# Kernel optimization log

Measured on AMD Instinct MI355X. Metric: run time of the kernel, lower is better.

Reference implementation:

```python
import jax, jax.numpy as jnp
import numpy as np

N_NODES = 100_000
E_OFF = 1_000_000
HID = 32
GF = 8
NF = 8
N_LAYERS = 3


def _mlp(h, W1, b1, W2, b2):
    # Linear -> ReLU -> Linear (matches MLP([in, hidden, out]))
    return jax.nn.relu(h @ W1 + b1) @ W2 + b2


def _seg_mean(v, idx, n):
    s = jax.ops.segment_sum(v, idx, num_segments=n)
    c = jax.ops.segment_sum(jnp.ones((v.shape[0], 1), v.dtype), idx, num_segments=n)
    return s / jnp.maximum(c, 1.0)


def _graphnet(x, row, col, eattr2, g, p):
    # GraphNet with global block: edge MLP -> mean-aggregate to nodes -> node MLP -> global MLP
    eW1, eb1, eW2, eb2, nW1, nb1, nW2, nb2, gW1, gb1, gW2, gb2 = p
    n, e = x.shape[0], row.shape[0]
    gE = jnp.broadcast_to(g, (e, g.shape[1]))
    e_emb = _mlp(jnp.concatenate([gE, x[row], x[col], eattr2], axis=1), eW1, eb1, eW2, eb2)
    agg = _seg_mean(e_emb, row, n)
    gN = jnp.broadcast_to(g, (n, g.shape[1]))
    n_emb = _mlp(jnp.concatenate([gN, x, agg], axis=1), nW1, nb1, nW2, nb2)
    g_new = _mlp(jnp.concatenate([n_emb.mean(0, keepdims=True), e_emb.mean(0, keepdims=True), g], axis=1),
                 gW1, gb1, gW2, gb2)
    return e_emb, n_emb, g_new


def setup_inputs() -> dict:
    key = jax.random.key(0)
    ks = jax.random.split(key, 24)
    a = jax.random.randint(ks[0], (E_OFF,), 0, N_NODES)
    b = jax.random.randint(ks[1], (E_OFF,), 0, N_NODES)
    d = jnp.arange(N_NODES)
    l_ei = jnp.stack([jnp.concatenate([jnp.maximum(a, b), d]),
                      jnp.concatenate([jnp.minimum(a, b), d])])  # lower triangular + diag
    c = jax.random.randint(ks[2], (E_OFF,), 0, N_NODES)
    e = jax.random.randint(ks[3], (E_OFF,), 0, N_NODES)
    u_ei = jnp.stack([jnp.concatenate([jnp.minimum(c, e), d]),
                      jnp.concatenate([jnp.maximum(c, e), d])])  # upper triangular + diag
    E = E_OFF + N_NODES
    x = jax.random.normal(ks[4], (N_NODES, NF), dtype=jnp.float32)
    l_attr = jax.random.normal(ks[5], (E, 1), dtype=jnp.float32)
    u_attr = jax.random.normal(ks[6], (E, 1), dtype=jnp.float32)

    def w(k, shape):
        return (jax.random.normal(k, shape, dtype=jnp.float32) / np.sqrt(shape[-2])).astype(jnp.float32)

    e_in = GF + 2 * NF + 1 + 1  # 26 (edge attr padded to 2: skip col, zeros where absent)
    n_in = GF + 1 + NF          # 17
    g_in = NF + 1 + GF          # 17
    return {
        'x': x, 'l_edge_index': l_ei, 'u_edge_index': u_ei,
        'l_edge_attr': l_attr, 'u_edge_attr': u_attr,
        'eW1': w(ks[7], (2, N_LAYERS, e_in, HID)), 'eb1': 0.01 * jax.random.normal(ks[8], (2, N_LAYERS, HID)),
        'eW2': w(ks[9], (2, N_LAYERS, HID, 1)), 'eb2': 0.01 * jax.random.normal(ks[10], (2, N_LAYERS, 1)),
        'nW1': w(ks[11], (2, N_LAYERS, n_in, HID)), 'nb1': 0.01 * jax.random.normal(ks[12], (2, N_LAYERS, HID)),
        'nW2': w(ks[13], (2, N_LAYERS, HID, NF)), 'nb2': 0.01 * jax.random.normal(ks[14], (2, N_LAYERS, NF)),
        'gW1': w(ks[15], (2, N_LAYERS, g_in, HID)), 'gb1': 0.01 * jax.random.normal(ks[16], (2, N_LAYERS, HID)),
        'gW2': w(ks[17], (2, N_LAYERS, HID, GF)), 'gb2': 0.01 * jax.random.normal(ks[18], (2, N_LAYERS, GF)),
    }


def reference(x, l_edge_index, u_edge_index, l_edge_attr, u_edge_attr,
              eW1, eb1, eW2, eb2, nW1, nb1, nW2, nb2, gW1, gb1, gW2, gb2):
    params = (eW1, eb1, eW2, eb2, nW1, nb1, nW2, nb2, gW1, gb1, gW2, gb2)
    lr, lc = l_edge_index[0], l_edge_index[1]
    ur, uc = u_edge_index[0], u_edge_index[1]
    g = jnp.zeros((1, GF), x.dtype)
    l_e, u_e = l_edge_attr, u_edge_attr
    l_a = l_edge_attr  # skip-connection edge features (original matrix values)
    zl, zu = jnp.zeros_like(l_edge_attr), jnp.zeros_like(u_edge_attr)
    for i in range(N_LAYERS):
        p1 = tuple(w[0, i] for w in params)
        p2 = tuple(w[1, i] for w in params)
        l_in = jnp.concatenate([l_e, l_a if i != 0 else zl], axis=1)  # zeros col == no skip (block 0)
        l_e, l_n, g = _graphnet(x, lr, lc, l_in, g, p1)
        u_in = jnp.concatenate([u_e, zu], axis=1)  # l2 never has skip; padded zeros col
        u_e, u_n, g = _graphnet(l_n, ur, uc, u_in, g, p2)
        # NOTE: node embeddings are NOT carried across MP blocks in the original
    l_vals = jnp.where(lr == lc, jnp.exp(l_e[:, 0]), l_e[:, 0])
    u_vals = jnp.where(ur == uc, jnp.exp(u_e[:, 0]), u_e[:, 0])
    return jnp.concatenate([l_vals, u_vals])
```

## Files before the change

kernel.cpp:

```cpp
#include <hip/hip_runtime.h>


typedef unsigned int u32;
typedef unsigned long long u64;

#define NB_SHIFT 8
#define NB_SIZE 256
#define RSTRIDE 1104

__device__ __forceinline__ float wave_sum(float v) {
#pragma unroll
    for (int off = 32; off > 0; off >>= 1) v += __shfl_down(v, off, 64);
    return v;
}


__global__ __launch_bounds__(512) void hist_kernel(
    const int* __restrict__ lr, const int* __restrict__ ur,
    u32* __restrict__ hist, int E, int B) {
    __shared__ u32 h[512];
    const int t = threadIdx.x;
    if (t < B) h[t] = 0;
    __syncthreads();
    const int s = blockIdx.y;
    const int* rows = s ? ur : lr;
    for (int i = blockIdx.x * 512 + t; i < E; i += gridDim.x * 512)
        atomicAdd(&h[rows[i] >> NB_SHIFT], 1u);
    __syncthreads();
    if (t < B && h[t]) atomicAdd(&hist[s * B + t], h[t]);
}

__global__ __launch_bounds__(512) void scan_kernel(
    const u32* __restrict__ hist, u32* __restrict__ offs,
    u32* __restrict__ cur, int B) {
    __shared__ u32 sh[512];
    const int t = threadIdx.x;
    for (int s = 0; s < 2; ++s) {
        const u32 v = (t < B) ? hist[s * B + t] : 0u;
        sh[t] = v;
        __syncthreads();
#pragma unroll
        for (int off = 1; off < 512; off <<= 1) {
            const u32 add = (t >= off) ? sh[t - off] : 0u;
            __syncthreads();
            sh[t] += add;
            __syncthreads();
        }
        const u32 exc = sh[t] - v;
        if (t < B) {
            offs[s * (B + 1) + t] = exc;
            cur[s * B + t] = exc;
        }
        if (t == 511) offs[s * (B + 1) + B] = sh[511];
        __syncthreads();
    }
}

#define SCHUNK 4096
__global__ __launch_bounds__(512) void scatter_kernel(
    const int* __restrict__ rows, const int* __restrict__ cols,
    const float* __restrict__ attr, u32* __restrict__ cur,
    uint4* __restrict__ my, int E, int B) {
    __shared__ u32 lcnt[512], lbase[512];
    const int t = threadIdx.x;
    if (t < B) lcnt[t] = 0;
    __syncthreads();
    const int base_e = blockIdx.x * SCHUNK;
#pragma unroll
    for (int k = 0; k < SCHUNK / 512; ++k) {
        const int e = base_e + k * 512 + t;
        if (e < E) atomicAdd(&lcnt[rows[e] >> NB_SHIFT], 1u);
    }
    __syncthreads();
    if (t < B) {
        const u32 c = lcnt[t];
        lbase[t] = c ? atomicAdd(&cur[t], c) : 0u;
        lcnt[t] = 0;
    }
    __syncthreads();
#pragma unroll
    for (int k = 0; k < SCHUNK / 512; ++k) {
        const int e = base_e + k * 512 + t;
        if (e < E) {
            const int r = rows[e];
            const int b = r >> NB_SHIFT;
            const u32 pos = lbase[b] + atomicAdd(&lcnt[b], 1u);
            my[pos] = make_uint4((u32)r, (u32)cols[e], (u32)e,
                                 __float_as_uint(attr[e]));
        }
    }
}


__global__ __launch_bounds__(512) void sort_kernel(
    const uint4* __restrict__ in, u64* __restrict__ okey,
    float* __restrict__ oattr, const u32* __restrict__ offs,
    u32* __restrict__ row_offs, int E, int N) {
    __shared__ u32 cnt[NB_SIZE];
    __shared__ u32 scn[NB_SIZE];
    const int t = threadIdx.x;
    const int b = blockIdx.x;
    const u32 beg = offs[b], end = offs[b + 1];
    if (t < NB_SIZE) cnt[t] = 0;
    __syncthreads();
    for (u32 i = beg + t; i < end; i += 512)
        atomicAdd(&cnt[in[i].x & (NB_SIZE - 1)], 1u);
    __syncthreads();
    if (t < NB_SIZE) scn[t] = cnt[t];
    __syncthreads();
#pragma unroll
    for (int off = 1; off < NB_SIZE; off <<= 1) {
        u32 add = 0;
        if (t < NB_SIZE && t >= off) add = scn[t - off];
        __syncthreads();
        if (t < NB_SIZE) scn[t] += add;
        __syncthreads();
    }
    const int n0 = b << NB_SHIFT;
    if (t < NB_SIZE) {
        const u32 excl = scn[t] - cnt[t];
        if (n0 + t < N) row_offs[n0 + t] = beg + excl;
        cnt[t] = excl;
    }
    if (b == 0 && t == 0) row_offs[N] = (u32)E;
    __syncthreads();
    for (u32 i = beg + t; i < end; i += 512) {
        const uint4 r = in[i];
        const u32 pos = beg + atomicAdd(&cnt[r.x & (NB_SIZE - 1)], 1u);
        okey[pos] = ((u64)r.z << 34) | ((u64)(r.x & 0x1FFFFu) << 17) |
                    (u64)(r.y & 0x1FFFFu);
        oattr[pos] = __uint_as_float(r.w);
    }
}


template <bool GCOMP>
__global__ __launch_bounds__(256) void nodew_kernel(
    const float4* __restrict__ xf, const float* __restrict__ W1,
    const float* __restrict__ b1,
    const float* __restrict__ gprev,
    float* __restrict__ gout,
    const float* __restrict__ pebins,
    const float* __restrict__ pnbins,
    const float* __restrict__ gW1, const float* __restrict__ gb1,
    const float* __restrict__ gW2, const float* __restrict__ gb2,
    float4* __restrict__ Atab, int N, float inv_E, int cpn) {
    __shared__ float gsh[8];
    const int t = threadIdx.x;
    if constexpr (GCOMP) {
        if (t < 64) {
            float nb[8];
#pragma unroll
            for (int q = 0; q < 8; ++q) nb[q] = pnbins[t * 16 + q];
            const float eb = pebins[t];
            float gin[17];
#pragma unroll
            for (int q = 0; q < 8; ++q) {
                const float s = wave_sum(nb[q]);
                gin[q] = __shfl(s, 0, 64) / (float)N;
            }
            const float es = wave_sum(eb);
            gin[8] = __shfl(es, 0, 64) * inv_E;
#pragma unroll
            for (int k = 0; k < 8; ++k) gin[9 + k] = gprev[k];
            float hv = 0.0f;
            if (t < 32) {
                hv = gb1[t];
#pragma unroll
                for (int k = 0; k < 17; ++k)
                    hv = fmaf(gin[k], gW1[k * 32 + t], hv);
                hv = fmaxf(hv, 0.0f);
            }
#pragma unroll
            for (int q = 0; q < 8; ++q) {
                const float c = (t < 32) ? hv * gW2[t * 8 + q] : 0.0f;
                const float s = wave_sum(c);
                if (t == 0) {
                    const float gv = gb2[q] + s;
                    gsh[q] = gv;
                    if (blockIdx.x == 0) gout[q] = gv;
                }
            }
        }
    } else {
        if (t < 8) gsh[t] = gprev[t];
    }
    __syncthreads();
    const int lid = (blockIdx.x & 7) * cpn + (blockIdx.x >> 3);
    const int n = lid * 256 + t;
    if (n >= N) return;
    float gr[8];
#pragma unroll
    for (int k = 0; k < 8; ++k) gr[k] = gsh[k];
    const float4 x0 = xf[2 * (size_t)n], x1 = xf[2 * (size_t)n + 1];
    const float xs[8] = {x0.x, x0.y, x0.z, x0.w, x1.x, x1.y, x1.z, x1.w};
    float a[32];
#pragma unroll
    for (int j = 0; j < 32; ++j) {
        float v = b1[j];
#pragma unroll
        for (int k = 0; k < 8; ++k) v = fmaf(gr[k], W1[k * 32 + j], v);
        a[j] = v;
    }
    const float* __restrict__ WA = W1 + 8 * 32;
#pragma unroll
    for (int k = 0; k < 8; ++k) {
        const float v = xs[k];
#pragma unroll
        for (int j = 0; j < 32; ++j) a[j] = fmaf(v, WA[k * 32 + j], a[j]);
    }
    float4* An = Atab + 8 * (size_t)n;
#pragma unroll
    for (int q = 0; q < 8; ++q)
        An[q] = make_float4(a[4 * q], a[4 * q + 1], a[4 * q + 2], a[4 * q + 3]);
}


template <bool SKIP, bool FIRST, bool GAGG, bool VALS, bool STORE>
__global__ __launch_bounds__(256) void edge_kernel(
    const u64* __restrict__ ekey,
    const float* __restrict__ eattr,
    const float4* __restrict__ Atab,
    const float4* __restrict__ xf,
    const float* __restrict__ eprev,
    const float* __restrict__ W1,
    const float* __restrict__ W2,
    const float* __restrict__ b2,
    float* __restrict__ ebins,
    float* __restrict__ e_out,
    float* __restrict__ vals_out,
    int E, int cpx) {
    __shared__ float wpart[4];
    const int t = threadIdx.x;
    const int lid = (blockIdx.x & 7) * cpx + (blockIdx.x >> 3);
    const int i0 = lid * 256;
    if (i0 >= E) return;
    const int i = i0 + t;
    const bool valid = i < E;
    const int idx = valid ? i : i0;

    const u64 key = ekey[idx];
    const u32 c = (u32)key & 0x1FFFFu;
    const u32 r = (u32)(key >> 17) & 0x1FFFFu;
    float attr = 0.0f;
    if constexpr (FIRST || SKIP) attr = eattr[idx];
    float epv;
    if constexpr (FIRST) epv = attr;
    else epv = eprev[idx];
    const float4* __restrict__ Ar = Atab + 8 * (size_t)r;
    float h[32];
#pragma unroll
    for (int q = 0; q < 8; ++q) {
        const float4 av = Ar[q];
        h[4 * q + 0] = av.x; h[4 * q + 1] = av.y;
        h[4 * q + 2] = av.z; h[4 * q + 3] = av.w;
    }
    const float4 xc0 = xf[2 * (size_t)c], xc1 = xf[2 * (size_t)c + 1];
    const float cx[8] = {xc0.x, xc0.y, xc0.z, xc0.w,
                         xc1.x, xc1.y, xc1.z, xc1.w};
    const float* __restrict__ Wc = W1 + 16 * 32;
#pragma unroll
    for (int k = 0; k < 8; ++k) {
        const float v = cx[k];
#pragma unroll
        for (int j = 0; j < 32; ++j) h[j] = fmaf(v, Wc[k * 32 + j], h[j]);
    }
    const float* __restrict__ W24 = W1 + 24 * 32;
#pragma unroll
    for (int j = 0; j < 32; ++j) h[j] = fmaf(epv, W24[j], h[j]);
    if constexpr (SKIP) {
        const float* __restrict__ W25 = W1 + 25 * 32;
#pragma unroll
        for (int j = 0; j < 32; ++j) h[j] = fmaf(attr, W25[j], h[j]);
    }
    float out = b2[0];
#pragma unroll
    for (int j = 0; j < 32; ++j) out = fmaf(fmaxf(h[j], 0.0f), W2[j], out);

    if (valid) {
        if constexpr (STORE) e_out[i] = out;
        if constexpr (VALS) {
            const u32 eid = (u32)(key >> 34);
            vals_out[eid] = (r == c) ? expf(out) : out;
        }
    }
    if constexpr (GAGG) {
        const float s = wave_sum(valid ? out : 0.0f);
        if ((t & 63) == 0) wpart[t >> 6] = s;
        __syncthreads();
        if (t == 0)
            atomicAdd(&ebins[lid & 63],
                      wpart[0] + wpart[1] + wpart[2] + wpart[3]);
    }
}


template <bool STORE_N>
__global__ __launch_bounds__(256) void nodemlp_kernel(
    const float* __restrict__ ep,
    const u32* __restrict__ row_offs,
    const float4* __restrict__ xf,
    const float* __restrict__ g,
    const float* __restrict__ nW1, const float* __restrict__ nb1,
    const float* __restrict__ nW2, const float* __restrict__ nb2,
    float* __restrict__ n_out,
    float* __restrict__ nbins,
    int N, int cpn) {
    __shared__ float biasN[32];
    __shared__ float npart[4][8];
    const int t = threadIdx.x;
    if (t < 32) {
        float v = nb1[t];
#pragma unroll
        for (int k = 0; k < 8; ++k) v = fmaf(g[k], nW1[k * 32 + t], v);
        biasN[t] = v;
    }
    __syncthreads();
    const int lid = (blockIdx.x & 7) * cpn + (blockIdx.x >> 3);
    const int n = lid * 256 + t;
    const bool active = n < N;
    const int idx = active ? n : (N - 1);
    const u32 beg = row_offs[idx], end = row_offs[idx + 1];
    float ssum = 0.0f;
    for (u32 i = beg; i < end; ++i) ssum += ep[i];
    const float agg = ssum / fmaxf((float)(end - beg), 1.0f);
    const float4 x0 = xf[2 * (size_t)idx], x1 = xf[2 * (size_t)idx + 1];
    float in[9] = {x0.x, x0.y, x0.z, x0.w, x1.x, x1.y, x1.z, x1.w, agg};
    float h[32];
#pragma unroll
    for (int j = 0; j < 8; ++j) {
        const float4 bb = reinterpret_cast<const float4*>(biasN)[j];
        h[4 * j + 0] = bb.x; h[4 * j + 1] = bb.y;
        h[4 * j + 2] = bb.z; h[4 * j + 3] = bb.w;
    }
    const float* __restrict__ Wk = nW1 + 8 * 32;
#pragma unroll
    for (int k = 0; k < 9; ++k) {
        const float v = in[k];
#pragma unroll
        for (int j = 0; j < 32; ++j) h[j] = fmaf(v, Wk[k * 32 + j], h[j]);
    }
    float o[8];
#pragma unroll
    for (int q = 0; q < 8; ++q) o[q] = nb2[q];
#pragma unroll
    for (int j = 0; j < 32; ++j) {
        const float hv = fmaxf(h[j], 0.0f);
#pragma unroll
        for (int q = 0; q < 8; ++q) o[q] = fmaf(hv, nW2[j * 8 + q], o[q]);
    }
    if constexpr (STORE_N) {
        if (active) {
            reinterpret_cast<float4*>(n_out)[2 * n] =
                make_float4(o[0], o[1], o[2], o[3]);
            reinterpret_cast<float4*>(n_out)[2 * n + 1] =
                make_float4(o[4], o[5], o[6], o[7]);
        }
    }
#pragma unroll
    for (int q = 0; q < 8; ++q) {
        const float s2 = wave_sum(active ? o[q] : 0.0f);
        if ((t & 63) == 0) npart[t >> 6][q] = s2;
    }
    __syncthreads();
    if (t < 8) {
        float a = 0.0f;
#pragma unroll
        for (int w = 0; w < 4; ++w) a += npart[w][t];
        atomicAdd(&nbins[(blockIdx.x & 63) * 16 + t], a);
    }
}

extern "C" void kernel_launch(void* const* d_in, const int* in_sizes, int n_in,
                              void* d_out, int out_size, void* d_ws,
                              size_t ws_size, hipStream_t stream) {
    const float* x = (const float*)d_in[0];
    const int* l_ei = (const int*)d_in[1];
    const int* u_ei = (const int*)d_in[2];
    const float* l_attr = (const float*)d_in[3];
    const float* u_attr = (const float*)d_in[4];
    const float* eW1 = (const float*)d_in[5];
    const float* eb1 = (const float*)d_in[6];
    const float* eW2 = (const float*)d_in[7];
    const float* eb2 = (const float*)d_in[8];
    const float* nW1 = (const float*)d_in[9];
    const float* nb1 = (const float*)d_in[10];
    const float* nW2 = (const float*)d_in[11];
    const float* nb2 = (const float*)d_in[12];
    const float* gW1 = (const float*)d_in[13];
    const float* gb1 = (const float*)d_in[14];
    const float* gW2 = (const float*)d_in[15];
    const float* gb2 = (const float*)d_in[16];

    const int E = in_sizes[3];
    const int N = in_sizes[0] / 8;
    const int B = (N + NB_SIZE - 1) >> NB_SHIFT;
    const int Ep = (E + 3) & ~3;

    u64* ekeys = (u64*)d_ws;
    float* eattrs = (float*)(ekeys + (size_t)2 * E);
    uint4* tmp = (uint4*)(eattrs + (size_t)2 * E);
    float* Atab = (float*)tmp;
    float* l_e = Atab + (size_t)32 * N;
    float* u_e = (float*)(tmp + (size_t)E);
    float* l_n = u_e + Ep;
    float* gslot = l_n + (size_t)8 * N;
    u32* hist = (u32*)(gslot + 56);
    float* dyn_all = (float*)(hist + 2 * B);
    u32* offs = (u32*)(dyn_all + 5 * RSTRIDE);
    u32* cur = offs + 2 * (B + 1);
    u32* row_offs = cur + 2 * B;

    const int* lr = l_ei;
    const int* lc = l_ei + E;
    const int* ur = u_ei;
    const int* uc = u_ei + E;
    const int sg = (E + SCHUNK - 1) / SCHUNK;
    const int ng = (N + 255) / 256;
    const int ngp = (ng + 7) & ~7;
    const int cpn = ngp >> 3;
    const int eg = (E + 255) / 256;
    const int nwg8 = (eg + 7) & ~7;
    const int cpx = nwg8 >> 3;
    const float invE = 1.0f / (float)E;
    float* outL = (float*)d_out;
    float* outU = outL + E;

    hipMemsetAsync(gslot, 0, (size_t)(56 + 2 * B + 5 * RSTRIDE) * sizeof(float),
                   stream);
    hist_kernel<<<dim3(64, 2), 512, 0, stream>>>(lr, ur, hist, E, B);
    scan_kernel<<<1, 512, 0, stream>>>(hist, offs, cur, B);
    scatter_kernel<<<sg, 512, 0, stream>>>(lr, lc, l_attr, cur, tmp, E, B);
    sort_kernel<<<B, 512, 0, stream>>>(tmp, ekeys, eattrs, offs, row_offs,
                                       E, N);
    scatter_kernel<<<sg, 512, 0, stream>>>(ur, uc, u_attr, cur + B, tmp, E, B);
    sort_kernel<<<B, 512, 0, stream>>>(tmp, ekeys + (size_t)E,
                                       eattrs + (size_t)E, offs + (B + 1),
                                       row_offs + (N + 1), E, N);

    const size_t wsl[6] = {0, 3, 1, 4, 2, 5};

    for (int j = 0; j < 6; ++j) {
        const bool lower = !(j & 1);
        const size_t sl = wsl[j];
        float* ebins = dyn_all + (size_t)(j <= 4 ? j : 4) * RSTRIDE;
        float* nbins = ebins + 64;
        const float* pe = (j >= 1) ? dyn_all + (size_t)(j - 1) * RSTRIDE : nullptr;
        const float* pn = (j >= 1) ? pe + 64 : nullptr;
        const size_t psl = (j >= 1) ? wsl[j - 1] : 0;
        const float4* exf = (const float4*)(lower ? x : l_n);
        const u64* ekey_t = ekeys + (size_t)(lower ? 0 : 1) * E;
        const float* eattr_t = eattrs + (size_t)(lower ? 0 : 1) * E;
        const u32* roffs = row_offs + (size_t)(lower ? 0 : 1) * (N + 1);
        const float* eprev = lower ? l_e : u_e;
        float* e_out = lower ? l_e : u_e;
        const float* gprev = gslot + (size_t)(j >= 1 ? j - 1 : 0) * 8;
        float* gout = gslot + (size_t)j * 8;

        if (j == 0)
            nodew_kernel<false><<<ngp, 256, 0, stream>>>(
                exf, eW1 + sl * 832, eb1 + sl * 32, gprev, gout, pe, pn,
                gW1, gb1, gW2, gb2, (float4*)Atab, N, invE, cpn);
        else
            nodew_kernel<true><<<ngp, 256, 0, stream>>>(
                exf, eW1 + sl * 832, eb1 + sl * 32, gprev, gout, pe, pn,
                gW1 + psl * 544, gb1 + psl * 32, gW2 + psl * 256,
                gb2 + psl * 8, (float4*)Atab, N, invE, cpn);

#define EDGE_ARGS                                                             \
    ekey_t, eattr_t, (const float4*)Atab, exf, eprev, eW1 + sl * 832,         \
        eW2 + sl * 32, eb2 + sl, ebins, e_out, (j == 4) ? outL : outU, E, cpx

        switch (j) {
            case 0: edge_kernel<false, true, true, false, true>
                        <<<nwg8, 256, 0, stream>>>(EDGE_ARGS); break;
            case 1: edge_kernel<false, true, true, false, true>
                        <<<nwg8, 256, 0, stream>>>(EDGE_ARGS); break;
            case 2: edge_kernel<true, false, true, false, true>
                        <<<nwg8, 256, 0, stream>>>(EDGE_ARGS); break;
            case 3: edge_kernel<false, false, true, false, true>
                        <<<nwg8, 256, 0, stream>>>(EDGE_ARGS); break;
            case 4: edge_kernel<true, false, true, true, true>
                        <<<nwg8, 256, 0, stream>>>(EDGE_ARGS); break;
            case 5: edge_kernel<false, false, false, true, false>
                        <<<nwg8, 256, 0, stream>>>(EDGE_ARGS); break;
        }
#undef EDGE_ARGS

        if (j == 5) break;

        const float4* nxf = (const float4*)(lower ? x : l_n);

#define NODE_ARGS                                                             \
    e_out, roffs, nxf, gslot + (size_t)j * 8, nW1 + sl * 544, nb1 + sl * 32,  \
        nW2 + sl * 256, nb2 + sl * 8, l_n, nbins, N, cpn

        switch (j) {
            case 0: nodemlp_kernel<true>
                        <<<ngp, 256, 0, stream>>>(NODE_ARGS); break;
            case 1: nodemlp_kernel<false>
                        <<<ngp, 256, 0, stream>>>(NODE_ARGS); break;
            case 2: nodemlp_kernel<true>
                        <<<ngp, 256, 0, stream>>>(NODE_ARGS); break;
            case 3: nodemlp_kernel<false>
                        <<<ngp, 256, 0, stream>>>(NODE_ARGS); break;
            case 4: nodemlp_kernel<true>
                        <<<ngp, 256, 0, stream>>>(NODE_ARGS); break;
        }
#undef NODE_ARGS
    }
}
```

Before: 515.9 us.

## Remove per-layer nodew kernel by precomputing x tables and fusing into edge/node kernels

The per-layer nodew kernel is removed. The global-MLP step and the g-dependent bias now run at the start of each edge kernel block, and the bias is added when the per-row table is loaded. The x-dependent row tables for the three lower layers are precomputed once by a new kernel. The upper-layer row table is written by the node MLP kernel in the same pass that produces l_n. This cuts six launches and one full N×32 table write/read pass per layer, at the cost of every edge block redundantly computing the global MLP and bias, plus extra workspace for three tables.

```diff
diff --git a/kernel.cpp b/kernel.cpp
--- a/kernel.cpp
+++ b/kernel.cpp
@@ -134,19 +134,62 @@
 }
 
 
-template <bool GCOMP>
-__global__ __launch_bounds__(256) void nodew_kernel(
-    const float4* __restrict__ xf, const float* __restrict__ W1,
+__global__ __launch_bounds__(256) void atabx_kernel(
+    const float4* __restrict__ xf, const float* __restrict__ eW1,
+    float4* __restrict__ AtabL, int N) {
+    const int n = blockIdx.x * 256 + threadIdx.x;
+    if (n >= N) return;
+    const float4 x0 = xf[2 * (size_t)n], x1 = xf[2 * (size_t)n + 1];
+    const float xs[8] = {x0.x, x0.y, x0.z, x0.w, x1.x, x1.y, x1.z, x1.w};
+    for (int m = 0; m < 3; ++m) {
+        const float* __restrict__ WA = eW1 + (size_t)m * 832 + 8 * 32;
+        float a[32];
+#pragma unroll
+        for (int j = 0; j < 32; ++j) a[j] = 0.0f;
+#pragma unroll
+        for (int k = 0; k < 8; ++k) {
+            const float v = xs[k];
+#pragma unroll
+            for (int j = 0; j < 32; ++j) a[j] = fmaf(v, WA[k * 32 + j], a[j]);
+        }
+        float4* An = AtabL + (size_t)m * 8 * N + 8 * (size_t)n;
+#pragma unroll
+        for (int q = 0; q < 8; ++q)
+            An[q] = make_float4(a[4 * q], a[4 * q + 1], a[4 * q + 2],
+                                a[4 * q + 3]);
+    }
+}
+
+
+template <bool SKIP, bool FIRST, bool GAGG, bool VALS, bool STORE, bool GCOMP>
+__global__ __launch_bounds__(256) void edge_kernel(
+    const u64* __restrict__ ekey,
+    const float* __restrict__ eattr,
+    const float4* __restrict__ Atab,
+    const float4* __restrict__ xf,
+    const float* __restrict__ eprev,
+    const float* __restrict__ W1,
     const float* __restrict__ b1,
+    const float* __restrict__ W2,
+    const float* __restrict__ b2,
     const float* __restrict__ gprev,
     float* __restrict__ gout,
     const float* __restrict__ pebins,
     const float* __restrict__ pnbins,
     const float* __restrict__ gW1, const float* __restrict__ gb1,
     const float* __restrict__ gW2, const float* __restrict__ gb2,
-    float4* __restrict__ Atab, int N, float inv_E, int cpn) {
+    float* __restrict__ ebins,
+    float* __restrict__ e_out,
+    float* __restrict__ vals_out,
+    int E, int N, float inv_E, int cpx) {
     __shared__ float gsh[8];
+    __shared__ float biasE[32];
+    __shared__ float wpart[4];
     const int t = threadIdx.x;
+    const int lid = (blockIdx.x & 7) * cpx + (blockIdx.x >> 3);
+    const int i0 = lid * 256;
+    if (i0 >= E) return;
+
     if constexpr (GCOMP) {
         if (t < 64) {
             float nb[8];
@@ -186,55 +229,14 @@
         if (t < 8) gsh[t] = gprev[t];
     }
     __syncthreads();
-    const int lid = (blockIdx.x & 7) * cpn + (blockIdx.x >> 3);
-    const int n = lid * 256 + t;
-    if (n >= N) return;
-    float gr[8];
-#pragma unroll
-    for (int k = 0; k < 8; ++k) gr[k] = gsh[k];
-    const float4 x0 = xf[2 * (size_t)n], x1 = xf[2 * (size_t)n + 1];
-    const float xs[8] = {x0.x, x0.y, x0.z, x0.w, x1.x, x1.y, x1.z, x1.w};
-    float a[32];
-#pragma unroll
-    for (int j = 0; j < 32; ++j) {
-        float v = b1[j];
-#pragma unroll
-        for (int k = 0; k < 8; ++k) v = fmaf(gr[k], W1[k * 32 + j], v);
-        a[j] = v;
-    }
-    const float* __restrict__ WA = W1 + 8 * 32;
-#pragma unroll
-    for (int k = 0; k < 8; ++k) {
-        const float v = xs[k];
-#pragma unroll
-        for (int j = 0; j < 32; ++j) a[j] = fmaf(v, WA[k * 32 + j], a[j]);
-    }
-    float4* An = Atab + 8 * (size_t)n;
-#pragma unroll
-    for (int q = 0; q < 8; ++q)
-        An[q] = make_float4(a[4 * q], a[4 * q + 1], a[4 * q + 2], a[4 * q + 3]);
-}
-
-
-template <bool SKIP, bool FIRST, bool GAGG, bool VALS, bool STORE>
-__global__ __launch_bounds__(256) void edge_kernel(
-    const u64* __restrict__ ekey,
-    const float* __restrict__ eattr,
-    const float4* __restrict__ Atab,
-    const float4* __restrict__ xf,
-    const float* __restrict__ eprev,
-    const float* __restrict__ W1,
-    const float* __restrict__ W2,
-    const float* __restrict__ b2,
-    float* __restrict__ ebins,
-    float* __restrict__ e_out,
-    float* __restrict__ vals_out,
-    int E, int cpx) {
-    __shared__ float wpart[4];
-    const int t = threadIdx.x;
-    const int lid = (blockIdx.x & 7) * cpx + (blockIdx.x >> 3);
-    const int i0 = lid * 256;
-    if (i0 >= E) return;
+    if (t < 32) {
+        float v = b1[t];
+#pragma unroll
+        for (int k = 0; k < 8; ++k) v = fmaf(gsh[k], W1[k * 32 + t], v);
+        biasE[t] = v;
+    }
+    __syncthreads();
+
     const int i = i0 + t;
     const bool valid = i < E;
     const int idx = valid ? i : i0;
@@ -252,8 +254,9 @@
 #pragma unroll
     for (int q = 0; q < 8; ++q) {
         const float4 av = Ar[q];
-        h[4 * q + 0] = av.x; h[4 * q + 1] = av.y;
-        h[4 * q + 2] = av.z; h[4 * q + 3] = av.w;
+        const float4 bi = reinterpret_cast<const float4*>(biasE)[q];
+        h[4 * q + 0] = bi.x + av.x; h[4 * q + 1] = bi.y + av.y;
+        h[4 * q + 2] = bi.z + av.z; h[4 * q + 3] = bi.w + av.w;
     }
     const float4 xc0 = xf[2 * (size_t)c], xc1 = xf[2 * (size_t)c + 1];
     const float cx[8] = {xc0.x, xc0.y, xc0.z, xc0.w,
@@ -295,7 +298,7 @@
 }
 
 
-template <bool STORE_N>
+template <bool EVEN>
 __global__ __launch_bounds__(256) void nodemlp_kernel(
     const float* __restrict__ ep,
     const u32* __restrict__ row_offs,
@@ -305,6 +308,8 @@
     const float* __restrict__ nW2, const float* __restrict__ nb2,
     float* __restrict__ n_out,
     float* __restrict__ nbins,
+    const float* __restrict__ W1u,
+    float4* __restrict__ AtabU,
     int N, int cpn) {
     __shared__ float biasN[32];
     __shared__ float npart[4][8];
@@ -349,12 +354,28 @@
 #pragma unroll
         for (int q = 0; q < 8; ++q) o[q] = fmaf(hv, nW2[j * 8 + q], o[q]);
     }
-    if constexpr (STORE_N) {
+    if constexpr (EVEN) {
         if (active) {
             reinterpret_cast<float4*>(n_out)[2 * n] =
                 make_float4(o[0], o[1], o[2], o[3]);
             reinterpret_cast<float4*>(n_out)[2 * n + 1] =
                 make_float4(o[4], o[5], o[6], o[7]);
+            const float* __restrict__ WA = W1u + 8 * 32;
+            float a[32];
+#pragma unroll
+            for (int j = 0; j < 32; ++j) a[j] = 0.0f;
+#pragma unroll
+            for (int k = 0; k < 8; ++k) {
+                const float v = o[k];
+#pragma unroll
+                for (int j = 0; j < 32; ++j)
+                    a[j] = fmaf(v, WA[k * 32 + j], a[j]);
+            }
+            float4* An = AtabU + 8 * (size_t)n;
+#pragma unroll
+            for (int q = 0; q < 8; ++q)
+                An[q] = make_float4(a[4 * q], a[4 * q + 1], a[4 * q + 2],
+                                    a[4 * q + 3]);
         }
     }
 #pragma unroll
@@ -400,9 +421,10 @@
     u64* ekeys = (u64*)d_ws;
     float* eattrs = (float*)(ekeys + (size_t)2 * E);
     uint4* tmp = (uint4*)(eattrs + (size_t)2 * E);
-    float* Atab = (float*)tmp;
-    float* l_e = Atab + (size_t)32 * N;
-    float* u_e = (float*)(tmp + (size_t)E);
+    float* AtabU = (float*)tmp;
+    float* l_e = AtabU + (size_t)32 * N;
+    float* AtabL = (float*)(tmp + (size_t)E);
+    float* u_e = AtabL + (size_t)96 * N;
     float* l_n = u_e + Ep;
     float* gslot = l_n + (size_t)8 * N;
     u32* hist = (u32*)(gslot + 56);
@@ -437,6 +459,8 @@
     sort_kernel<<<B, 512, 0, stream>>>(tmp, ekeys + (size_t)E,
                                        eattrs + (size_t)E, offs + (B + 1),
                                        row_offs + (N + 1), E, N);
+    atabx_kernel<<<ng, 256, 0, stream>>>((const float4*)x, eW1,
+                                         (float4*)AtabL, N);
 
     const size_t wsl[6] = {0, 3, 1, 4, 2, 5};
 
@@ -456,44 +480,37 @@
         float* e_out = lower ? l_e : u_e;
         const float* gprev = gslot + (size_t)(j >= 1 ? j - 1 : 0) * 8;
         float* gout = gslot + (size_t)j * 8;
-
-        if (j == 0)
-            nodew_kernel<false><<<ngp, 256, 0, stream>>>(
-                exf, eW1 + sl * 832, eb1 + sl * 32, gprev, gout, pe, pn,
-                gW1, gb1, gW2, gb2, (float4*)Atab, N, invE, cpn);
-        else
-            nodew_kernel<true><<<ngp, 256, 0, stream>>>(
-                exf, eW1 + sl * 832, eb1 + sl * 32, gprev, gout, pe, pn,
-                gW1 + psl * 544, gb1 + psl * 32, gW2 + psl * 256,
-                gb2 + psl * 8, (float4*)Atab, N, invE, cpn);
+        const float* Atab_j =
+            lower ? AtabL + (size_t)(j >> 1) * 32 * N : AtabU;
 
 #define EDGE_ARGS                                                             \
-    ekey_t, eattr_t, (const float4*)Atab, exf, eprev, eW1 + sl * 832,         \
-        eW2 + sl * 32, eb2 + sl, ebins, e_out, (j == 4) ? outL : outU, E, cpx
+    ekey_t, eattr_t, (const float4*)Atab_j, exf, eprev, eW1 + sl * 832,       \
+        eb1 + sl * 32, eW2 + sl * 32, eb2 + sl, gprev, gout, pe, pn,          \
+        gW1 + psl * 544, gb1 + psl * 32, gW2 + psl * 256, gb2 + psl * 8,      \
+        ebins, e_out, (j == 4) ? outL : outU, E, N, invE, cpx
 
         switch (j) {
-            case 0: edge_kernel<false, true, true, false, true>
+            case 0: edge_kernel<false, true, true, false, true, false>
                         <<<nwg8, 256, 0, stream>>>(EDGE_ARGS); break;
-            case 1: edge_kernel<false, true, true, false, true>
+            case 1: edge_kernel<false, true, true, false, true, true>
                         <<<nwg8, 256, 0, stream>>>(EDGE_ARGS); break;
-            case 2: edge_kernel<true, false, true, false, true>
+            case 2: edge_kernel<true, false, true, false, true, true>
                         <<<nwg8, 256, 0, stream>>>(EDGE_ARGS); break;
-            case 3: edge_kernel<false, false, true, false, true>
+            case 3: edge_kernel<false, false, true, false, true, true>
                         <<<nwg8, 256, 0, stream>>>(EDGE_ARGS); break;
-            case 4: edge_kernel<true, false, true, true, true>
+            case 4: edge_kernel<true, false, true, true, true, true>
                         <<<nwg8, 256, 0, stream>>>(EDGE_ARGS); break;
-            case 5: edge_kernel<false, false, false, true, false>
+            case 5: edge_kernel<false, false, false, true, false, true>
                         <<<nwg8, 256, 0, stream>>>(EDGE_ARGS); break;
         }
 #undef EDGE_ARGS
 
         if (j == 5) break;
 
-        const float4* nxf = (const float4*)(lower ? x : l_n);
-
 #define NODE_ARGS                                                             \
-    e_out, roffs, nxf, gslot + (size_t)j * 8, nW1 + sl * 544, nb1 + sl * 32,  \
-        nW2 + sl * 256, nb2 + sl * 8, l_n, nbins, N, cpn
+    e_out, roffs, exf, gslot + (size_t)j * 8, nW1 + sl * 544, nb1 + sl * 32,  \
+        nW2 + sl * 256, nb2 + sl * 8, l_n, nbins,                             \
+        eW1 + wsl[j + 1] * 832, (float4*)AtabU, N, cpn
 
         switch (j) {
             case 0: nodemlp_kernel<true>
```

After: 503.6 us. -2.4%, faster.
